# Kernel optimization log

Hardware: AMD Instinct MI355X
Metric: run time of the kernel (lower is better)

## Reference

```python
import math
import jax, jax.numpy as jnp
import numpy as np

N_HEAD = 16
HEAD_DIM = 128


def _rope(x, cos, sin):
    # x: (B,T,H,D); cos,sin: (T,1,D/2) broadcast over B,H
    d = x.shape[-1] // 2
    x1, x2 = x[..., :d], x[..., d:]
    return jnp.concatenate([x1 * cos + x2 * sin, -x1 * sin + x2 * cos], axis=-1)


def _rms_norm(x, eps=1e-6):
    return x * jax.lax.rsqrt(jnp.mean(x * x, axis=-1, keepdims=True) + eps)


def setup_inputs() -> dict:
    key = jax.random.key(0)
    ks = jax.random.split(key, 9)
    B, T, C = 2, 2048, 2048
    scale = 1.0 / math.sqrt(C)
    return {
        "x": jax.random.normal(ks[0], (B, T, C), jnp.float32),
        "ve": jax.random.normal(ks[1], (B, T, C), jnp.float32),
        "Wq": jax.random.normal(ks[2], (C, C), jnp.float32) * scale,
        "Wk": jax.random.normal(ks[3], (C, C), jnp.float32) * scale,
        "Wv": jax.random.normal(ks[4], (C, C), jnp.float32) * scale,
        "Wproj": jax.random.normal(ks[5], (C, C), jnp.float32) * scale,
        "Wgate": jax.random.normal(ks[6], (N_HEAD, 12), jnp.float32) * (1.0 / math.sqrt(12.0)),
        "cos": jax.random.uniform(ks[7], (T, 1, HEAD_DIM // 2), jnp.float32),
        "sin": jax.random.uniform(ks[8], (T, 1, HEAD_DIM // 2), jnp.float32),
        "window_left": 1024,
    }


def reference(x, ve, Wq, Wk, Wv, Wproj, Wgate, cos, sin, window_left):
    B, T, C = x.shape
    H, D = N_HEAD, HEAD_DIM

    # Linear projections (torch Linear: x @ W.T)
    q = (x @ Wq.T).reshape(B, T, H, D)
    k = (x @ Wk.T).reshape(B, T, H, D)
    v = (x @ Wv.T).reshape(B, T, H, D)

    # value-embedding gating (has_ve layer)
    gate = 3.0 * jax.nn.sigmoid(x[..., :12] @ Wgate.T)  # (B,T,H)
    v = v + gate[..., None] * ve.reshape(B, T, H, D)

    # rope + qk rms-norm * 1.2
    q = _rms_norm(_rope(q, cos, sin)) * 1.2
    k = _rms_norm(_rope(k, cos, sin)) * 1.2

    # windowed causal mask
    row = jnp.arange(T)[:, None]
    col = jnp.arange(T)[None, :]
    mask = row >= col
    if 0 < window_left < T:
        mask = mask & (row - col <= window_left)
    bias = jnp.where(mask, 0.0, -1e9).astype(x.dtype)  # (T,T)

    scale = 1.0 / math.sqrt(D)
    att = jnp.einsum("bqhd,bkhd->bhqk", q, k) * scale + bias[None, None]
    att = jax.nn.softmax(att, axis=-1)
    y = jnp.einsum("bhqk,bkhd->bqhd", att, v).reshape(B, T, H * D)
    return y @ Wproj.T
```

## Files before the change

### kernel.cpp

```cpp
#include <hip/hip_runtime.h>
#include <hip/hip_bf16.h>
#include <cstdint>

#define N_HEAD 16
#define HEAD_DIM 128

typedef __bf16 bf16;
typedef __bf16 bf16x8 __attribute__((ext_vector_type(8)));
typedef __bf16 bf16x4 __attribute__((ext_vector_type(4)));
typedef float f32x4 __attribute__((ext_vector_type(4)));

__device__ __forceinline__ void gload_lds16(const void* g, void* l) {
  auto gp = reinterpret_cast<const __attribute__((address_space(1))) char*>(
      reinterpret_cast<uintptr_t>(g));
  auto lp = reinterpret_cast<__attribute__((address_space(3))) char*>(
      reinterpret_cast<uintptr_t>(l));
  __builtin_amdgcn_global_load_lds(gp, lp, 16, 0, 0);
}

__global__ __launch_bounds__(256) void cvt_all(
    const float* __restrict__ x, const float* __restrict__ Wq,
    const float* __restrict__ Wk, const float* __restrict__ Wv,
    const float* __restrict__ Wp, bf16* __restrict__ xb,
    bf16* __restrict__ wqkv, bf16* __restrict__ wpb, int nx4, int nw4) {
  const int z = blockIdx.z;
  const float* in;
  bf16* out;
  int n4;
  if (z == 0)      { in = x;  out = xb;  n4 = nx4; }
  else if (z == 1) { in = Wq; out = wqkv;                     n4 = nw4; }
  else if (z == 2) { in = Wk; out = wqkv + (size_t)nw4 * 4;   n4 = nw4; }
  else if (z == 3) { in = Wv; out = wqkv + (size_t)nw4 * 8;   n4 = nw4; }
  else             { in = Wp; out = wpb;  n4 = nw4; }
  const int i = blockIdx.x * 256 + threadIdx.x;
  if (i >= n4) return;
  const float4 f = reinterpret_cast<const float4*>(in)[i];
  bf16x4 o;
  o.x = (bf16)f.x; o.y = (bf16)f.y; o.z = (bf16)f.z; o.w = (bf16)f.w;
  reinterpret_cast<bf16x4*>(out)[i] = o;
}

template <typename OutT>
__global__ __launch_bounds__(256) void gemm_bt(
    const bf16* __restrict__ A, const bf16* __restrict__ Bt,
    OutT* __restrict__ C, int M, int N, int K) {
  __shared__ __align__(16) bf16 As[2][128 * 32];
  __shared__ __align__(16) bf16 Bs[2][128 * 32];
  const int tid = threadIdx.x;
  const int lane = tid & 63;
  const int wave = tid >> 6;
  const int wm = (wave >> 1) * 64;
  const int wn = (wave & 1) * 64;
  const int lr = lane & 15;
  const int lk = (lane >> 4) * 8;

  const bf16* Ab = A + (size_t)blockIdx.y * 128 * K;
  const bf16* Bb = Bt + (size_t)blockIdx.x * 128 * K;

  const int r0 = tid >> 2;
  const int c0 = (tid & 3) * 8;

  f32x4 acc[4][4] = {};

  for (int k0 = 0; k0 < K; k0 += 64) {
    __syncthreads();
#pragma unroll
    for (int s = 0; s < 2; ++s) {
      const int kk = k0 + s * 32 + c0;
      gload_lds16(Ab + (size_t)r0 * K + kk, As[s] + (size_t)tid * 8);
      gload_lds16(Ab + (size_t)(r0 + 64) * K + kk, As[s] + (size_t)(256 + tid) * 8);
      gload_lds16(Bb + (size_t)r0 * K + kk, Bs[s] + (size_t)tid * 8);
      gload_lds16(Bb + (size_t)(r0 + 64) * K + kk, Bs[s] + (size_t)(256 + tid) * 8);
    }
    __syncthreads();

#pragma unroll
    for (int s = 0; s < 2; ++s) {
      bf16x8 a[4], b[4];
#pragma unroll
      for (int i = 0; i < 4; ++i)
        a[i] = *reinterpret_cast<const bf16x8*>(As[s] + (wm + i * 16 + lr) * 32 + lk);
#pragma unroll
      for (int j = 0; j < 4; ++j)
        b[j] = *reinterpret_cast<const bf16x8*>(Bs[s] + (wn + j * 16 + lr) * 32 + lk);
#pragma unroll
      for (int i = 0; i < 4; ++i)
#pragma unroll
        for (int j = 0; j < 4; ++j)
          acc[i][j] = __builtin_amdgcn_mfma_f32_16x16x32_bf16(a[i], b[j], acc[i][j], 0, 0, 0);
    }
  }

  const int orow = blockIdx.y * 128 + wm + (lane >> 4) * 4;
  const int ocol = blockIdx.x * 128 + wn + lr;
#pragma unroll
  for (int i = 0; i < 4; ++i)
#pragma unroll
    for (int j = 0; j < 4; ++j)
#pragma unroll
      for (int r = 0; r < 4; ++r)
        C[(size_t)(orow + i * 16 + r) * N + (ocol + j * 16)] = (OutT)acc[i][j][r];
}

__global__ __launch_bounds__(512, 2) void gemm256(
    const bf16* __restrict__ A, const bf16* __restrict__ Bt,
    bf16* __restrict__ C, int M, int N, int K) {
  __shared__ __align__(16) char sA[2][32768];
  __shared__ __align__(16) char sB[2][32768];

  const int nwgy = M >> 8;
  const int nwg = (N >> 8) * nwgy;
  const int q8 = nwg >> 3;
  const int wgid = (blockIdx.x & 7) * q8 + (blockIdx.x >> 3);
  const int by = wgid % nwgy;
  const int bx = wgid / nwgy;

  const int tid = threadIdx.x;
  const int lane = tid & 63;
  const int wave = tid >> 6;
  const int wm = (wave >> 2) << 7;
  const int wn = (wave & 3) << 6;
  const int lr = lane & 15;
  const int lk16 = (lane >> 4) << 4;
  const int sx = (lr & 7) << 4;

  const bf16* Ab = A + (size_t)by * 256 * K;
  const bf16* Bb = Bt + (size_t)bx * 256 * K;

  int srow[2], scol[2];
#pragma unroll
  for (int pp = 0; pp < 2; ++pp) {
    const int o = pp * 8192 + tid * 16;
    srow[pp] = o >> 7;
    scol[pp] = (o & 127) ^ ((srow[pp] & 7) << 4);
  }

  auto stageA = [&](int buf, int half, int k0) {
#pragma unroll
    for (int pp = 0; pp < 2; ++pp)
      gload_lds16(Ab + (size_t)(half * 128 + srow[pp]) * K + k0 + (scol[pp] >> 1),
                  sA[buf] + half * 16384 + pp * 8192 + tid * 16);
  };
  auto stageB = [&](int buf, int half, int k0) {
#pragma unroll
    for (int pp = 0; pp < 2; ++pp)
      gload_lds16(Bb + (size_t)(half * 128 + srow[pp]) * K + k0 + (scol[pp] >> 1),
                  sB[buf] + half * 16384 + pp * 8192 + tid * 16);
  };

  f32x4 acc[8][4] = {};
  bf16x8 bF[4][2];

#define VMCNT4                                             \
  asm volatile("s_waitcnt vmcnt(4)" ::: "memory");         \
  __builtin_amdgcn_sched_barrier(0)
#define VMCNT0                                             \
  asm volatile("s_waitcnt vmcnt(0)" ::: "memory");         \
  __builtin_amdgcn_sched_barrier(0)

#define PHASE(BUF, P, STAGE, WAIT)                                             \
  {                                                                            \
    bf16x8 aF[2][2];                                                           \
    if (P == 0) {                                                              \
      _Pragma("unroll") for (int n = 0; n < 4; ++n)                            \
      _Pragma("unroll") for (int ks = 0; ks < 2; ++ks)                         \
        bF[n][ks] = *reinterpret_cast<const bf16x8*>(                          \
            sB[BUF] + (wn + n * 16 + lr) * 128 + ((ks * 64 + lk16) ^ sx));     \
    }                                                                          \
    _Pragma("unroll") for (int mi = 0; mi < 2; ++mi)                           \
    _Pragma("unroll") for (int ks = 0; ks < 2; ++ks)                           \
      aF[mi][ks] = *reinterpret_cast<const bf16x8*>(                           \
          sA[BUF] + (wm + (P * 2 + mi) * 16 + lr) * 128 +                      \
          ((ks * 64 + lk16) ^ sx));                                            \
    STAGE;                                                                     \
    WAIT;                                                                      \
    __builtin_amdgcn_s_barrier();                                              \
    __builtin_amdgcn_s_setprio(1);                                             \
    _Pragma("unroll") for (int ks = 0; ks < 2; ++ks)                           \
    _Pragma("unroll") for (int mi = 0; mi < 2; ++mi)                           \
    _Pragma("unroll") for (int n = 0; n < 4; ++n)                              \
      acc[P * 2 + mi][n] = __builtin_amdgcn_mfma_f32_16x16x32_bf16(            \
          aF[mi][ks], bF[n][ks], acc[P * 2 + mi][n], 0, 0, 0);                 \
    __builtin_amdgcn_s_setprio(0);                                             \
    __builtin_amdgcn_s_barrier();                                              \
  }

  const int nIt = K >> 7;

  stageB(0, 0, 0); stageB(0, 1, 0);
  stageA(0, 0, 0); stageA(0, 1, 0);
  stageB(1, 0, 64); stageB(1, 1, 64);
  VMCNT4;
  __builtin_amdgcn_s_barrier();

  int k0 = 0;
  for (int it = 0; it < nIt - 1; ++it, k0 += 128) {
    PHASE(0, 0, stageA(1, 0, k0 + 64), );
    PHASE(0, 1, stageA(1, 1, k0 + 64), );
    PHASE(0, 2, stageB(0, 0, k0 + 128), );
    PHASE(0, 3, stageB(0, 1, k0 + 128), VMCNT4);
    PHASE(1, 0, stageA(0, 0, k0 + 128), );
    PHASE(1, 1, stageA(0, 1, k0 + 128), );
    PHASE(1, 2, stageB(1, 0, k0 + 192), );
    PHASE(1, 3, stageB(1, 1, k0 + 192), VMCNT4);
  }
  PHASE(0, 0, stageA(1, 0, k0 + 64), );
  PHASE(0, 1, stageA(1, 1, k0 + 64), );
  PHASE(0, 2, , );
  PHASE(0, 3, , VMCNT0);
  PHASE(1, 0, , );
  PHASE(1, 1, , );
  PHASE(1, 2, , );
  PHASE(1, 3, , );
#undef PHASE
#undef VMCNT4
#undef VMCNT0

  const int orow = by * 256 + wm + (lane >> 4) * 4;
  const int ocol = bx * 256 + wn + lr;
#pragma unroll
  for (int m = 0; m < 8; ++m)
#pragma unroll
    for (int n = 0; n < 4; ++n)
#pragma unroll
      for (int r = 0; r < 4; ++r)
        C[(size_t)(orow + m * 16 + r) * N + (ocol + n * 16)] = (bf16)acc[m][n][r];
}

__global__ __launch_bounds__(256) void rope_rms(
    bf16* __restrict__ qkv, const float* __restrict__ cs,
    const float* __restrict__ sn, int T) {
  const int C = N_HEAD * HEAD_DIM;
  const int S = 3 * C;
  const int bt = blockIdx.x;
  const int t = bt % T;
  const int wave = threadIdx.x >> 6;
  const int lane = threadIdx.x & 63;
  const int h = blockIdx.y * 4 + wave;
  bf16* p = qkv + (size_t)bt * S + (blockIdx.z ? C : 0) + h * HEAD_DIM;
  const float oscale = blockIdx.z ? 1.2f : 0.15302091809294977f;
  const float c = cs[t * 64 + lane];
  const float s = sn[t * 64 + lane];
  const float x1 = (float)p[lane];
  const float x2 = (float)p[lane + 64];
  const float r1 = x1 * c + x2 * s;
  const float r2 = x2 * c - x1 * s;
  float ss = r1 * r1 + r2 * r2;
#pragma unroll
  for (int m = 1; m < 64; m <<= 1) ss += __shfl_xor(ss, m);
  const float sc = oscale * rsqrtf(ss * (1.0f / 128.0f) + 1e-6f);
  p[lane] = (bf16)(r1 * sc);
  p[lane + 64] = (bf16)(r2 * sc);
}

__global__ __launch_bounds__(256) void gate_transpose(
    const bf16* __restrict__ qkv, const float* __restrict__ x,
    const float* __restrict__ ve, const float* __restrict__ Wg,
    bf16* __restrict__ vT, int T) {
  const int C = N_HEAD * HEAD_DIM;
  const int S = 3 * C;
  const int t0 = blockIdx.x * 64;
  const int c0 = blockIdx.y * 64;
  const int b = blockIdx.z;
  const int h = c0 >> 7;

  __shared__ float gs[64];
  __shared__ __align__(16) bf16 tile[64][72];

  if (threadIdx.x < 64) {
    const float* xr = x + (size_t)(b * T + t0 + threadIdx.x) * C;
    float a = 0.f;
#pragma unroll
    for (int j = 0; j < 12; ++j) a += xr[j] * Wg[h * 12 + j];
    gs[threadIdx.x] = 3.f / (1.f + __expf(-a));
  }
  __syncthreads();

  {
    const int r = threadIdx.x >> 2;
    const int cc = (threadIdx.x & 3) * 16;
    const size_t vrow = (size_t)(b * T + t0 + r) * S + 2 * C + c0 + cc;
    const size_t erow = (size_t)(b * T + t0 + r) * C + c0 + cc;
    bf16x8 a0 = *reinterpret_cast<const bf16x8*>(qkv + vrow);
    bf16x8 a1 = *reinterpret_cast<const bf16x8*>(qkv + vrow + 8);
    const float g = gs[r];
    bf16x8 o0, o1;
#pragma unroll
    for (int i = 0; i < 8; ++i) o0[i] = (bf16)((float)a0[i] + g * ve[erow + i]);
#pragma unroll
    for (int i = 0; i < 8; ++i) o1[i] = (bf16)((float)a1[i] + g * ve[erow + 8 + i]);
    *reinterpret_cast<bf16x8*>(&tile[r][cc]) = o0;
    *reinterpret_cast<bf16x8*>(&tile[r][cc + 8]) = o1;
  }
  __syncthreads();
  {
    const int dr = threadIdx.x >> 2;
    const int tc = (threadIdx.x & 3) * 16;
    bf16x8 o0, o1;
#pragma unroll
    for (int i = 0; i < 8; ++i) o0[i] = tile[tc + i][dr];
#pragma unroll
    for (int i = 0; i < 8; ++i) o1[i] = tile[tc + 8 + i][dr];
    const size_t orow =
        ((size_t)((b * N_HEAD + h) * HEAD_DIM) + (c0 & 127) + dr) * T + t0 + tc;
    *reinterpret_cast<bf16x8*>(vT + orow) = o0;
    *reinterpret_cast<bf16x8*>(vT + orow + 8) = o1;
  }
}

__global__ __launch_bounds__(256, 2) void attn(
    const bf16* __restrict__ qkv, const bf16* __restrict__ vT,
    bf16* __restrict__ y, const int* __restrict__ wptr, int T, int B) {
  const int C = N_HEAD * HEAD_DIM;
  const int S = 3 * C;
  const int nq = T >> 7;
  const int ppx = (B * N_HEAD) >> 3;
  const int bid = blockIdx.x;
  const int xcd = bid & 7;
  const int sl = bid >> 3;
  const int pair = xcd * ppx + sl / nq;
  const int qi = sl % nq;
  const int b = pair / N_HEAD;
  const int h = pair % N_HEAD;
  const int qb = qi * 128;

  const int tid = threadIdx.x;
  const int wave = tid >> 6;
  const int lane = tid & 63;
  const int lm = lane & 15;
  const int quad = lane >> 4;

  const int w = wptr[0];
  const int W = (w > 0 && w < T) ? w : (1 << 30);

  __shared__ __align__(16) bf16 Ks[4][64][32];
  __shared__ __align__(16) bf16 Vs[2][128][32];
  __shared__ __align__(16) bf16 Pb[4][16][72];

  const bf16* kb = qkv + (size_t)b * T * S + C + (size_t)h * HEAD_DIM;
  const bf16* vb = vT + (size_t)((b * N_HEAD + h) * HEAD_DIM) * T;

  const int qt[2] = {qb + wave * 16, qb + 64 + wave * 16};
  bf16x8 qf[2][4];
#pragma unroll
  for (int t = 0; t < 2; ++t) {
    const bf16* qrow = qkv + (size_t)(b * T + qt[t] + lm) * S + h * HEAD_DIM;
#pragma unroll
    for (int c = 0; c < 4; ++c)
      qf[t][c] = *reinterpret_cast<const bf16x8*>(qrow + c * 32 + quad * 8);
  }

  float mrun[2] = {-1e30f, -1e30f}, lrun[2] = {0.f, 0.f};
  f32x4 oacc[2][8] = {};

  int kstart = qb - W;
  if (kstart < 0) kstart = 0;
  kstart &= ~63;
  const int kend = qb + 64;

  const int sr = tid >> 2;
  const int sc = (tid & 3) * 8;

  bf16x8 kpre[4], vpre[4];
  {
    const bf16* kr = kb + (size_t)(kstart + sr) * S + sc;
#pragma unroll
    for (int c = 0; c < 4; ++c)
      kpre[c] = *reinterpret_cast<const bf16x8*>(kr + c * 32);
#pragma unroll
    for (int c2 = 0; c2 < 2; ++c2)
#pragma unroll
      for (int i = 0; i < 2; ++i)
        vpre[c2 * 2 + i] = *reinterpret_cast<const bf16x8*>(
            vb + (size_t)(i * 64 + sr) * T + kstart + c2 * 32 + sc);
  }

  for (int kc = kstart; kc <= kend; kc += 64) {
    __syncthreads();
#pragma unroll
    for (int c = 0; c < 4; ++c)
      *reinterpret_cast<bf16x8*>(&Ks[c][sr][sc]) = kpre[c];
#pragma unroll
    for (int c2 = 0; c2 < 2; ++c2)
#pragma unroll
      for (int i = 0; i < 2; ++i)
        *reinterpret_cast<bf16x8*>(&Vs[c2][i * 64 + sr][sc]) = vpre[c2 * 2 + i];
    __syncthreads();

    if (kc + 64 <= kend) {
      const int kc2 = kc + 64;
      const bf16* kr = kb + (size_t)(kc2 + sr) * S + sc;
#pragma unroll
      for (int c = 0; c < 4; ++c)
        kpre[c] = *reinterpret_cast<const bf16x8*>(kr + c * 32);
#pragma unroll
      for (int c2 = 0; c2 < 2; ++c2)
#pragma unroll
        for (int i = 0; i < 2; ++i)
          vpre[c2 * 2 + i] = *reinterpret_cast<const bf16x8*>(
              vb + (size_t)(i * 64 + sr) * T + kc2 + c2 * 32 + sc);
    }

#pragma unroll
    for (int t = 0; t < 2; ++t) {
      const int q0 = qt[t];
      if (kc > q0 + 15 || kc + 63 < q0 - W) continue;
      const int qr = q0 + lm;

      f32x4 st[4] = {};
#pragma unroll
      for (int g = 0; g < 4; ++g)
#pragma unroll
        for (int c = 0; c < 4; ++c) {
          const bf16x8 kf =
              *reinterpret_cast<const bf16x8*>(&Ks[c][g * 16 + lm][quad * 8]);
          st[g] = __builtin_amdgcn_mfma_f32_16x16x32_bf16(kf, qf[t][c], st[g], 0, 0, 0);
        }
      float mx = -1e30f;
#pragma unroll
      for (int g = 0; g < 4; ++g)
#pragma unroll
        for (int r = 0; r < 4; ++r) {
          const int key = kc + g * 16 + quad * 4 + r;
          const bool valid = (key <= qr) && (qr - key <= W);
          st[g][r] = valid ? st[g][r] : -1e30f;
          mx = fmaxf(mx, st[g][r]);
        }
      mx = fmaxf(mx, __shfl_xor(mx, 16));
      mx = fmaxf(mx, __shfl_xor(mx, 32));
      const float mnew = fmaxf(mrun[t], mx);
      const float alpha = __builtin_amdgcn_exp2f(mrun[t] - mnew);
      mrun[t] = mnew;
      float rs = 0.f;
#pragma unroll
      for (int g = 0; g < 4; ++g) {
        bf16x4 pk;
#pragma unroll
        for (int r = 0; r < 4; ++r) {
          const float p = __builtin_amdgcn_exp2f(st[g][r] - mnew);
          rs += p;
          pk[r] = (bf16)p;
        }
        *reinterpret_cast<bf16x4*>(&Pb[wave][lm][g * 16 + quad * 4]) = pk;
      }
      rs += __shfl_xor(rs, 16);
      rs += __shfl_xor(rs, 32);
      lrun[t] = lrun[t] * alpha + rs;
#pragma unroll
      for (int dc = 0; dc < 8; ++dc)
#pragma unroll
        for (int r = 0; r < 4; ++r) oacc[t][dc][r] *= alpha;
#pragma unroll
      for (int c2 = 0; c2 < 2; ++c2) {
        const bf16x8 pf =
            *reinterpret_cast<const bf16x8*>(&Pb[wave][lm][c2 * 32 + quad * 8]);
#pragma unroll
        for (int dc = 0; dc < 8; ++dc) {
          const bf16x8 vf =
              *reinterpret_cast<const bf16x8*>(&Vs[c2][dc * 16 + lm][quad * 8]);
          oacc[t][dc] = __builtin_amdgcn_mfma_f32_16x16x32_bf16(vf, pf, oacc[t][dc], 0, 0, 0);
        }
      }
    }
  }

#pragma unroll
  for (int t = 0; t < 2; ++t) {
    const float inv = 1.f / lrun[t];
    bf16* yr = y + (size_t)(b * T + qt[t] + lm) * C + h * HEAD_DIM;
#pragma unroll
    for (int dc = 0; dc < 8; ++dc) {
      bf16x4 o;
#pragma unroll
      for (int r = 0; r < 4; ++r) o[r] = (bf16)(oacc[t][dc][r] * inv);
      *reinterpret_cast<bf16x4*>(yr + dc * 16 + quad * 4) = o;
    }
  }
}

extern "C" void kernel_launch(void* const* d_in, const int* in_sizes, int n_in,
                              void* d_out, int out_size, void* d_ws, size_t ws_size,
                              hipStream_t stream) {
  const float* x  = (const float*)d_in[0];
  const float* ve = (const float*)d_in[1];
  const float* Wq = (const float*)d_in[2];
  const float* Wk = (const float*)d_in[3];
  const float* Wv = (const float*)d_in[4];
  const float* Wp = (const float*)d_in[5];
  const float* Wg = (const float*)d_in[6];
  const float* cs = (const float*)d_in[7];
  const float* sn = (const float*)d_in[8];
  const int*   wl = (const int*)d_in[9];
  float* out = (float*)d_out;

  const int C = N_HEAD * HEAD_DIM;
  const int T = in_sizes[7] / (HEAD_DIM / 2);
  const int B = in_sizes[0] / (T * C);
  const int M = B * T;

  bf16* xb   = (bf16*)d_ws;
  bf16* wqkv = xb   + (size_t)M * C;
  bf16* wpb  = wqkv + (size_t)3 * C * C;
  bf16* qkv  = wpb  + (size_t)C * C;
  bf16* ybuf = qkv  + (size_t)3 * M * C;
  bf16* vTb  = xb;

  const int nx4 = M * C / 4, nw4 = C * C / 4;
  cvt_all<<<dim3((nx4 + 255) / 256, 1, 5), 256, 0, stream>>>(
      x, Wq, Wk, Wv, Wp, xb, wqkv, wpb, nx4, nw4);

  gemm256<<<dim3((3 * C / 256) * (M / 256)), 512, 0, stream>>>(
      xb, wqkv, qkv, M, 3 * C, C);

  rope_rms<<<dim3(M, N_HEAD / 4, 2), 256, 0, stream>>>(qkv, cs, sn, T);
  gate_transpose<<<dim3(T / 64, C / 64, B), 256, 0, stream>>>(qkv, x, ve, Wg, vTb, T);
  attn<<<dim3(B * N_HEAD * (T / 128)), 256, 0, stream>>>(qkv, vTb, ybuf, wl, T, B);

  gemm_bt<float><<<dim3(C / 128, M / 128), 256, 0, stream>>>(ybuf, wpb, out, M, C, C);
}
```

Measured before the change: 418.6 us.

## Add pipelined 128x256 GEMM for output projection and split QKV GEMM tail

Introduces a new gemm128 kernel with 128x256 tiles, swizzled LDS, direct-to-LDS staged double buffering and phase-interleaved MFMA scheduling. It replaces the simple gemm_bt kernel for the output projection, and it also computes the V portion of the QKV GEMM so gemm256 only handles Q and K. The aim is better MFMA pipelining in the projection and better wave balance across CUs. The cost is an extra kernel launch and more complex hand-scheduled wait counts.

```diff
diff --git a/kernel.cpp b/kernel.cpp
--- a/kernel.cpp
+++ b/kernel.cpp
@@ -40,68 +40,6 @@
   reinterpret_cast<bf16x4*>(out)[i] = o;
 }
 
-template <typename OutT>
-__global__ __launch_bounds__(256) void gemm_bt(
-    const bf16* __restrict__ A, const bf16* __restrict__ Bt,
-    OutT* __restrict__ C, int M, int N, int K) {
-  __shared__ __align__(16) bf16 As[2][128 * 32];
-  __shared__ __align__(16) bf16 Bs[2][128 * 32];
-  const int tid = threadIdx.x;
-  const int lane = tid & 63;
-  const int wave = tid >> 6;
-  const int wm = (wave >> 1) * 64;
-  const int wn = (wave & 1) * 64;
-  const int lr = lane & 15;
-  const int lk = (lane >> 4) * 8;
-
-  const bf16* Ab = A + (size_t)blockIdx.y * 128 * K;
-  const bf16* Bb = Bt + (size_t)blockIdx.x * 128 * K;
-
-  const int r0 = tid >> 2;
-  const int c0 = (tid & 3) * 8;
-
-  f32x4 acc[4][4] = {};
-
-  for (int k0 = 0; k0 < K; k0 += 64) {
-    __syncthreads();
-#pragma unroll
-    for (int s = 0; s < 2; ++s) {
-      const int kk = k0 + s * 32 + c0;
-      gload_lds16(Ab + (size_t)r0 * K + kk, As[s] + (size_t)tid * 8);
-      gload_lds16(Ab + (size_t)(r0 + 64) * K + kk, As[s] + (size_t)(256 + tid) * 8);
-      gload_lds16(Bb + (size_t)r0 * K + kk, Bs[s] + (size_t)tid * 8);
-      gload_lds16(Bb + (size_t)(r0 + 64) * K + kk, Bs[s] + (size_t)(256 + tid) * 8);
-    }
-    __syncthreads();
-
-#pragma unroll
-    for (int s = 0; s < 2; ++s) {
-      bf16x8 a[4], b[4];
-#pragma unroll
-      for (int i = 0; i < 4; ++i)
-        a[i] = *reinterpret_cast<const bf16x8*>(As[s] + (wm + i * 16 + lr) * 32 + lk);
-#pragma unroll
-      for (int j = 0; j < 4; ++j)
-        b[j] = *reinterpret_cast<const bf16x8*>(Bs[s] + (wn + j * 16 + lr) * 32 + lk);
-#pragma unroll
-      for (int i = 0; i < 4; ++i)
-#pragma unroll
-        for (int j = 0; j < 4; ++j)
-          acc[i][j] = __builtin_amdgcn_mfma_f32_16x16x32_bf16(a[i], b[j], acc[i][j], 0, 0, 0);
-    }
-  }
-
-  const int orow = blockIdx.y * 128 + wm + (lane >> 4) * 4;
-  const int ocol = blockIdx.x * 128 + wn + lr;
-#pragma unroll
-  for (int i = 0; i < 4; ++i)
-#pragma unroll
-    for (int j = 0; j < 4; ++j)
-#pragma unroll
-      for (int r = 0; r < 4; ++r)
-        C[(size_t)(orow + i * 16 + r) * N + (ocol + j * 16)] = (OutT)acc[i][j][r];
-}
-
 __global__ __launch_bounds__(512, 2) void gemm256(
     const bf16* __restrict__ A, const bf16* __restrict__ Bt,
     bf16* __restrict__ C, int M, int N, int K) {
@@ -109,7 +47,7 @@
   __shared__ __align__(16) char sB[2][32768];
 
   const int nwgy = M >> 8;
-  const int nwg = (N >> 8) * nwgy;
+  const int nwg = gridDim.x;
   const int q8 = nwg >> 3;
   const int wgid = (blockIdx.x & 7) * q8 + (blockIdx.x >> 3);
   const int by = wgid % nwgy;
@@ -227,6 +165,128 @@
         C[(size_t)(orow + m * 16 + r) * N + (ocol + n * 16)] = (bf16)acc[m][n][r];
 }
 
+template <typename OutT>
+__global__ __launch_bounds__(512, 2) void gemm128(
+    const bf16* __restrict__ A, const bf16* __restrict__ Bt,
+    OutT* __restrict__ C, int M, int Ncols, int K, int nOff) {
+  __shared__ __align__(16) char sA[2][16384];
+  __shared__ __align__(16) char sB[2][32768];
+
+  const int nwgy = M >> 7;
+  const int nwg = gridDim.x;
+  const int q8 = nwg >> 3;
+  const int wgid = (blockIdx.x & 7) * q8 + (blockIdx.x >> 3);
+  const int by = wgid % nwgy;
+  const int bx = wgid / nwgy;
+
+  const int tid = threadIdx.x;
+  const int lane = tid & 63;
+  const int wave = tid >> 6;
+  const int wn = wave << 5;
+  const int lr = lane & 15;
+  const int lk16 = (lane >> 4) << 4;
+  const int sx = (lr & 7) << 4;
+
+  const bf16* Ab = A + (size_t)by * 128 * K;
+  const bf16* Bb = Bt + (size_t)(nOff + bx * 256) * K;
+
+  int srow[2], scol[2];
+#pragma unroll
+  for (int pp = 0; pp < 2; ++pp) {
+    const int o = pp * 8192 + tid * 16;
+    srow[pp] = o >> 7;
+    scol[pp] = (o & 127) ^ ((srow[pp] & 7) << 4);
+  }
+
+  auto stageB = [&](int buf, int half, int k0) {
+#pragma unroll
+    for (int pp = 0; pp < 2; ++pp)
+      gload_lds16(Bb + (size_t)(half * 128 + srow[pp]) * K + k0 + (scol[pp] >> 1),
+                  sB[buf] + half * 16384 + pp * 8192 + tid * 16);
+  };
+  auto stageA = [&](int buf, int half, int k0) {
+    const int o = tid * 16;
+    const int row = o >> 7;
+    const int col = (o & 127) ^ ((row & 7) << 4);
+    gload_lds16(Ab + (size_t)(half * 64 + row) * K + k0 + (col >> 1),
+                sA[buf] + half * 8192 + o);
+  };
+
+  f32x4 acc[8][2] = {};
+  bf16x8 bF[2][2];
+
+#define WAITV(n)                                               \
+  asm volatile("s_waitcnt vmcnt(" #n ")" ::: "memory");        \
+  __builtin_amdgcn_sched_barrier(0)
+
+#define PH128(BUF, P, STAGE, WAIT)                                             \
+  {                                                                            \
+    bf16x8 aF[2][2];                                                           \
+    if (P == 0) {                                                              \
+      _Pragma("unroll") for (int n = 0; n < 2; ++n)                            \
+      _Pragma("unroll") for (int ks = 0; ks < 2; ++ks)                         \
+        bF[n][ks] = *reinterpret_cast<const bf16x8*>(                          \
+            sB[BUF] + (wn + n * 16 + lr) * 128 + ((ks * 64 + lk16) ^ sx));     \
+    }                                                                          \
+    _Pragma("unroll") for (int mi = 0; mi < 2; ++mi)                           \
+    _Pragma("unroll") for (int ks = 0; ks < 2; ++ks)                           \
+      aF[mi][ks] = *reinterpret_cast<const bf16x8*>(                           \
+          sA[BUF] + ((P * 2 + mi) * 16 + lr) * 128 + ((ks * 64 + lk16) ^ sx)); \
+    STAGE;                                                                     \
+    WAIT;                                                                      \
+    __builtin_amdgcn_s_barrier();                                              \
+    __builtin_amdgcn_s_setprio(1);                                             \
+    _Pragma("unroll") for (int ks = 0; ks < 2; ++ks)                           \
+    _Pragma("unroll") for (int mi = 0; mi < 2; ++mi)                           \
+    _Pragma("unroll") for (int n = 0; n < 2; ++n)                              \
+      acc[P * 2 + mi][n] = __builtin_amdgcn_mfma_f32_16x16x32_bf16(            \
+          aF[mi][ks], bF[n][ks], acc[P * 2 + mi][n], 0, 0, 0);                 \
+    __builtin_amdgcn_s_setprio(0);                                             \
+    __builtin_amdgcn_s_barrier();                                              \
+  }
+
+  const int nIt = K >> 7;
+
+  stageB(0, 0, 0); stageB(0, 1, 0);
+  stageA(0, 0, 0); stageA(0, 1, 0);
+  stageB(1, 0, 64); stageB(1, 1, 64);
+  stageA(1, 0, 64);
+  WAITV(5);
+  __builtin_amdgcn_s_barrier();
+
+  int k0 = 0;
+  for (int it = 0; it < nIt - 1; ++it, k0 += 128) {
+    PH128(0, 0, stageA(1, 1, k0 + 64), );
+    PH128(0, 1, stageB(0, 0, k0 + 128), WAITV(8));
+    PH128(0, 2, (stageB(0, 1, k0 + 128), stageA(0, 0, k0 + 128)), );
+    PH128(0, 3, , WAITV(6));
+    PH128(1, 0, stageA(0, 1, k0 + 128), );
+    PH128(1, 1, stageB(1, 0, k0 + 192), WAITV(8));
+    PH128(1, 2, (stageB(1, 1, k0 + 192), stageA(1, 0, k0 + 192)), );
+    PH128(1, 3, , WAITV(6));
+  }
+  PH128(0, 0, stageA(1, 1, k0 + 64), );
+  PH128(0, 1, , WAITV(6));
+  PH128(0, 2, , );
+  PH128(0, 3, , WAITV(1));
+  PH128(1, 0, , );
+  PH128(1, 1, , WAITV(0));
+  PH128(1, 2, , );
+  PH128(1, 3, , );
+#undef PH128
+#undef WAITV
+
+  const int orow = by * 128 + (lane >> 4) * 4;
+  const int ocol = nOff + bx * 256 + wn + lr;
+#pragma unroll
+  for (int m = 0; m < 8; ++m)
+#pragma unroll
+    for (int n = 0; n < 2; ++n)
+#pragma unroll
+      for (int r = 0; r < 4; ++r)
+        C[(size_t)(orow + m * 16 + r) * Ncols + (ocol + n * 16)] = (OutT)acc[m][n][r];
+}
+
 __global__ __launch_bounds__(256) void rope_rms(
     bf16* __restrict__ qkv, const float* __restrict__ cs,
     const float* __restrict__ sn, int T) {
@@ -509,12 +569,14 @@
   cvt_all<<<dim3((nx4 + 255) / 256, 1, 5), 256, 0, stream>>>(
       x, Wq, Wk, Wv, Wp, xb, wqkv, wpb, nx4, nw4);
 
-  gemm256<<<dim3((3 * C / 256) * (M / 256)), 512, 0, stream>>>(
-      xb, wqkv, qkv, M, 3 * C, C);
+  gemm256<<<dim3((M / 256) * 16), 512, 0, stream>>>(xb, wqkv, qkv, M, 3 * C, C);
+  gemm128<bf16><<<dim3((M / 128) * 8), 512, 0, stream>>>(
+      xb, wqkv, qkv, M, 3 * C, C, 2 * C);
 
   rope_rms<<<dim3(M, N_HEAD / 4, 2), 256, 0, stream>>>(qkv, cs, sn, T);
   gate_transpose<<<dim3(T / 64, C / 64, B), 256, 0, stream>>>(qkv, x, ve, Wg, vTb, T);
   attn<<<dim3(B * N_HEAD * (T / 128)), 256, 0, stream>>>(qkv, vTb, ybuf, wl, T, B);
 
-  gemm_bt<float><<<dim3(C / 128, M / 128), 256, 0, stream>>>(ybuf, wpb, out, M, C, C);
-}
+  gemm128<float><<<dim3((M / 128) * (C / 256)), 512, 0, stream>>>(
+      ybuf, wpb, out, M, C, C, 0);
+}
```

New measurement: 395.8 us. 5.4% less time.
